# Kernel tuning notes

Measured on AMD Instinct MI355X. Metric: run time of the kernel, lower is better.

## Reference

```python
import jax, jax.numpy as jnp
import numpy as np

H = 128  # GRU hidden size


def _conv(x, w, b, stride):
    # x: NCHW, w: OIHW, VALID padding (torch Conv2d default padding=0)
    y = jax.lax.conv_general_dilated(x, w, (stride, stride), 'VALID',
                                     dimension_numbers=('NCHW', 'OIHW', 'NCHW'))
    return y + b[None, :, None, None]


def setup_inputs() -> dict:
    key = jax.random.key(0)
    ks = jax.random.split(key, 16)
    T, B, A = 128, 32, 6
    x = jax.random.uniform(ks[0], (T * B, 1, 84, 84), jnp.float32) * 255.0
    done = (jax.random.uniform(ks[1], (T * B,)) < 0.1).astype(jnp.float32)
    gru_state = jnp.zeros((1, B, H), jnp.float32)
    s = 0.05
    params = dict(
        conv1_w=jax.random.normal(ks[2], (32, 1, 8, 8)) * s,
        conv1_b=jnp.zeros((32,)),
        conv2_w=jax.random.normal(ks[3], (64, 32, 4, 4)) * s,
        conv2_b=jnp.zeros((64,)),
        conv3_w=jax.random.normal(ks[4], (64, 64, 3, 3)) * s,
        conv3_b=jnp.zeros((64,)),
        fc_w=jax.random.normal(ks[5], (512, 64 * 7 * 7)) * 0.02,
        fc_b=jnp.zeros((512,)),
        w_ih=jax.random.normal(ks[6], (3 * H, 512)) * 0.04,
        w_hh=jax.random.normal(ks[7], (3 * H, H)) * 0.08,
        b_ih=jnp.zeros((3 * H,)),
        b_hh=jnp.zeros((3 * H,)),
        actor_w=jax.random.normal(ks[8], (A, H)) * 0.01,
        actor_b=jnp.zeros((A,)),
        critic_w=jax.random.normal(ks[9], (1, H)) * 0.09,
        critic_b=jnp.zeros((1,)),
    )
    return dict(x=x, done=done, gru_state=gru_state, **params)


def reference(x, done, gru_state,
              conv1_w, conv1_b, conv2_w, conv2_b, conv3_w, conv3_b,
              fc_w, fc_b, w_ih, w_hh, b_ih, b_hh,
              actor_w, actor_b, critic_w, critic_b):
    # CNN encoder on x/255
    h = jax.nn.relu(_conv(x / 255.0, conv1_w, conv1_b, 4))  # [N,32,20,20]
    h = jax.nn.relu(_conv(h, conv2_w, conv2_b, 2))          # [N,64,9,9]
    h = jax.nn.relu(_conv(h, conv3_w, conv3_b, 1))          # [N,64,7,7]
    feat = jax.nn.relu(h.reshape(h.shape[0], -1) @ fc_w.T + fc_b)  # [N,512]

    B = gru_state.shape[1]
    feat = feat.reshape(-1, B, feat.shape[-1])  # [T,B,512]
    d = done.reshape(-1, B)                     # [T,B]

    # hoist input-to-gate projection out of the scan
    gx = jnp.einsum('tbi,gi->tbg', feat, w_ih) + b_ih  # [T,B,3H]

    def step(hprev, inp):
        gxt, dt = inp
        hprev = (1.0 - dt)[:, None] * hprev  # done-reset mask
        gh = hprev @ w_hh.T + b_hh           # [B,3H]
        r = jax.nn.sigmoid(gxt[:, :H] + gh[:, :H])
        z = jax.nn.sigmoid(gxt[:, H:2 * H] + gh[:, H:2 * H])
        n = jnp.tanh(gxt[:, 2 * H:] + r * gh[:, 2 * H:])
        hnew = (1.0 - z) * n + z * hprev
        return hnew, hnew

    h_final, hs = jax.lax.scan(step, gru_state[0], (gx, d))
    hidden = hs.reshape(-1, H)  # [T*B,H]

    logits = hidden @ actor_w.T + actor_b   # [N,A]
    value = hidden @ critic_w.T + critic_b  # [N,1]
    return logits, value, h_final[None]
```

## Files before the change

### kernel.cpp

```cpp
#include <hip/hip_runtime.h>
#include <hip/hip_bf16.h>
#include <stdint.h>

#define DI __device__ __forceinline__

typedef __bf16 bf16x8 __attribute__((ext_vector_type(8)));
typedef __bf16 bf16x4 __attribute__((ext_vector_type(4)));
typedef float f32x16 __attribute__((ext_vector_type(16)));

DI float bf2f(unsigned short u){ return __uint_as_float(((unsigned int)u)<<16); }
DI unsigned short f2bf(float f){
  unsigned int x = __float_as_uint(f);
  x += 0x7fffu + ((x>>16)&1u);
  return (unsigned short)(x>>16);
}
DI float sigmoidf_(float x){ return 1.0f/(1.0f + __expf(-x)); }

DI void gld_lds16(const void* g, void* l){
  __builtin_amdgcn_global_load_lds((const __attribute__((address_space(1))) void*)g,
                                   (__attribute__((address_space(3))) void*)l, 16, 0, 0);
}
DI f32x16 mfma32(bf16x8 a, bf16x8 b, f32x16 c){
  return __builtin_amdgcn_mfma_f32_32x32x16_bf16(a, b, c, 0, 0, 0);
}

__global__ __launch_bounds__(256) void k_prep_w1(const float* __restrict__ w1, unsigned short* __restrict__ o){
  int idx = blockIdx.x*256 + threadIdx.x;
  int j=idx&7, l=(idx>>3)&63, kk=idx>>9;
  int oc=l&31, kg=kk*16+((l>>5)<<3)+j;
  o[idx] = f2bf(w1[oc*64 + kg] * (1.0f/255.0f));
}
__global__ __launch_bounds__(256) void k_prep_w2(const float* __restrict__ w2, unsigned short* __restrict__ o){
  int idx = blockIdx.x*256 + threadIdx.x;
  int j=idx&7, l=(idx>>3)&63, nt=(idx>>9)&1, kh=(idx>>10)&1, s=idx>>11;
  int oc=nt*32+(l&31), ic=kh*16+(l>>5)*8+j, ky=s>>2, kx=s&3;
  o[idx] = f2bf(w2[((oc*32+ic)*4+ky)*4+kx]);
}
__global__ __launch_bounds__(256) void k_prep_w3(const float* __restrict__ w3, unsigned short* __restrict__ o){
  int idx = blockIdx.x*256 + threadIdx.x;
  int j=idx&7, l=(idx>>3)&63, nt=(idx>>9)&1, kh=(idx>>10)&3, s=idx>>12;
  int oc=nt*32+(l&31), ic=kh*16+(l>>5)*8+j, ky=s/3, kx=s-ky*3;
  o[idx] = f2bf(w3[((oc*64+ic)*3+ky)*3+kx]);
}
__global__ __launch_bounds__(512) void k_prep_fc(const float* __restrict__ fcw, unsigned short* __restrict__ o){
  int tid=threadIdx.x, ks=blockIdx.x, nt=blockIdx.y;
  int j=tid&7, l=tid>>3;
  int n=nt*32+(l&31), k=ks*16+(l>>5)*8+j;
  int c=k&63, pos=k>>6;
  float wv = fcw[(size_t)n*3136 + c*49 + pos];
  unsigned short hi = f2bf(wv);
  int idx = (nt*196+ks)*512 + tid;
  o[idx] = hi;
  o[1605632 + idx] = f2bf(wv - bf2f(hi));
}
__global__ __launch_bounds__(512) void k_prep_gx(const float* __restrict__ wih, unsigned short* __restrict__ o){
  int tid=threadIdx.x, ks=blockIdx.x, nt=blockIdx.y;
  int j=tid&7, l=tid>>3;
  int n=nt*32+(l&31), k=ks*16+(l>>5)*8+j;
  float wv = wih[(size_t)n*512 + k];
  unsigned short hi = f2bf(wv);
  int idx = (nt*32+ks)*512 + tid;
  o[idx] = hi;
  o[196608 + idx] = f2bf(wv - bf2f(hi));
}

__global__ __launch_bounds__(256) void k_conv1(const float* __restrict__ x,
    const unsigned short* __restrict__ w1p, const float* __restrict__ b,
    unsigned short* __restrict__ a1, int nbase)
{
  __shared__ __align__(16) char imgs[4*14784];
  const int tid=threadIdx.x, l=tid&63, w=tid>>6;
  const int nloc = blockIdx.x*4 + w;
  char* myimg = imgs + w*14784;
  const float* xp = x + (size_t)(nbase+nloc)*7056;

  for (int it=0; it<28; ++it){
    int idx4 = l + it*64;
    if (idx4 < 1764){
      float4 v = *(const float4*)(xp + idx4*4);
      int row = idx4/21, rem = idx4 - row*21;
      ushort4 u; u.x=f2bf(v.x); u.y=f2bf(v.y); u.z=f2bf(v.z); u.w=f2bf(v.w);
      *(ushort4*)(myimg + row*176 + rem*8) = u;
    }
  }

  bf16x8 wb[4];
  #pragma unroll
  for (int kk=0;kk<4;kk++) wb[kk] = *(const bf16x8*)(w1p + (kk*64 + l)*8);
  const float bias = b[l&31];
  asm volatile("s_waitcnt lgkmcnt(0)" ::: "memory");

  const int kyh = (l>>5);
  unsigned short* obase = a1 + (size_t)nloc*12800;
  for (int mt=0; mt<13; ++mt){
    int p = mt*32 + (l&31);
    p = min(p, 399);
    const int oy = p/20, ox = p - oy*20;
    const int rbyte = oy*4*176 + ox*8;
    f32x16 acc = {};
    #pragma unroll
    for (int kk=0;kk<4;kk++){
      const int a = rbyte + (kk*2 + kyh)*176;
      bf16x8 af;
      *(bf16x4*)&af       = *(const bf16x4*)(myimg + a);
      *((bf16x4*)&af + 1) = *(const bf16x4*)(myimg + a + 8);
      acc = mfma32(af, wb[kk], acc);
    }
    const int oc = l&31;
    #pragma unroll
    for (int rg=0;rg<16;rg++){
      int row = (rg&3) + 8*(rg>>2) + 4*kyh;
      int pos = mt*32 + row;
      if (pos < 400)
        obase[pos*32 + oc] = f2bf(fmaxf(acc[rg] + bias, 0.f));
    }
  }
}

__global__ __launch_bounds__(256) void k_conv2(const unsigned short* __restrict__ a1,
    const unsigned short* __restrict__ w2p, const float* __restrict__ b2,
    unsigned short* __restrict__ a2, int nbase)
{
  extern __shared__ __align__(16) char smem[];
  const int tid=threadIdx.x, l=tid&63, w=tid>>6;
  const int nloc = blockIdx.x*4 + w;
  char* myimg = smem + w*25600;
  const char* gimg = (const char*)(a1 + (size_t)nloc*12800);
  #pragma unroll
  for (int i=0;i<25;i++){
    int o = i*1024 + l*16;
    int q = o ^ (((o>>7)&7)<<4);
    gld_lds16(gimg + q, myimg + i*1024);
  }
  __syncthreads();
  int rbase[3];
  #pragma unroll
  for (int mt=0;mt<3;mt++){
    int r = mt*32 + (l&31);
    int oy=r/9, ox=r-oy*9;
    rbase[mt] = 40*oy + 2*ox;
  }
  const int grp16 = (l>>5)*16;
  f32x16 acc[3][2] = {};
  #pragma unroll
  for (int ky=0;ky<4;ky++){
    #pragma unroll
    for (int kx=0;kx<4;kx++){
      const int s = ky*4+kx;
      #pragma unroll
      for (int kh=0;kh<2;kh++){
        bf16x8 b0 = *(const bf16x8*)(w2p + (((s*2+kh)*2+0)*64 + l)*8);
        bf16x8 b1 = *(const bf16x8*)(w2p + (((s*2+kh)*2+1)*64 + l)*8);
        #pragma unroll
        for (int mt=0;mt<3;mt++){
          int ip = rbase[mt] + ky*20 + kx;
          ip = min(ip, 399);
          int byte = (ip*64 + kh*32 + grp16) ^ (((ip>>1)&7)<<4);
          bf16x8 af = *(const bf16x8*)(myimg + byte);
          acc[mt][0] = mfma32(af, b0, acc[mt][0]);
          acc[mt][1] = mfma32(af, b1, acc[mt][1]);
        }
      }
    }
  }
  const float bias0 = b2[l&31], bias1 = b2[32+(l&31)];
  unsigned short* ob = (unsigned short*)myimg;
  #pragma unroll
  for (int mt=0;mt<3;mt++){
    #pragma unroll
    for (int rg=0;rg<16;rg++){
      int r = mt*32 + (rg&3) + 8*(rg>>2) + 4*(l>>5);
      ob[r*64 + (l&31)]      = f2bf(fmaxf(acc[mt][0][rg]+bias0,0.f));
      ob[r*64 + 32 + (l&31)] = f2bf(fmaxf(acc[mt][1][rg]+bias1,0.f));
    }
  }
  asm volatile("s_waitcnt lgkmcnt(0)" ::: "memory");
  const uint4* s4 = (const uint4*)ob;
  uint4* d4 = (uint4*)(a2 + (size_t)(nbase+nloc)*5184);
  #pragma unroll
  for (int i=0;i<11;i++){
    int c = i*64 + l;
    if (c < 648) d4[c] = s4[c];
  }
}

__global__ __launch_bounds__(256) void k_conv3(const unsigned short* __restrict__ a2,
    const unsigned short* __restrict__ w3p, const float* __restrict__ b3,
    unsigned short* __restrict__ a3)
{
  __shared__ __align__(16) char smem3[4*11264];
  const int tid=threadIdx.x, l=tid&63, w=tid>>6;
  const int n = blockIdx.x*4 + w;
  char* myimg = smem3 + w*11264;
  const char* gimg = (const char*)(a2 + (size_t)n*5184);
  #pragma unroll
  for (int i=0;i<11;i++){
    int c = i*64 + l;
    int cc = min(c, 647);
    int o = cc*16;
    int q = o ^ (((o>>7)&7)<<4);
    gld_lds16(gimg + q, myimg + i*1024);
  }
  __syncthreads();
  int base[2];
  #pragma unroll
  for (int mt=0;mt<2;mt++){
    int r = mt*32 + (l&31);
    int oy=r/7, ox=r-oy*7;
    base[mt] = oy*9 + ox;
  }
  const int grp16 = (l>>5)*16;
  f32x16 acc[2][2] = {};
  #pragma unroll
  for (int ky=0;ky<3;ky++){
    #pragma unroll
    for (int kx=0;kx<3;kx++){
      const int s = ky*3+kx;
      #pragma unroll
      for (int kh=0;kh<4;kh++){
        bf16x8 b0 = *(const bf16x8*)(w3p + (((s*4+kh)*2+0)*64 + l)*8);
        bf16x8 b1 = *(const bf16x8*)(w3p + (((s*4+kh)*2+1)*64 + l)*8);
        #pragma unroll
        for (int mt=0;mt<2;mt++){
          int ip = min(base[mt] + ky*9 + kx, 80);
          int byte = (ip*128 + kh*32 + grp16) ^ ((ip&7)<<4);
          bf16x8 af = *(const bf16x8*)(myimg + byte);
          acc[mt][0] = mfma32(af, b0, acc[mt][0]);
          acc[mt][1] = mfma32(af, b1, acc[mt][1]);
        }
      }
    }
  }
  const float bias0 = b3[l&31], bias1 = b3[32+(l&31)];
  unsigned short* ob = (unsigned short*)myimg;
  #pragma unroll
  for (int mt=0;mt<2;mt++){
    #pragma unroll
    for (int rg=0;rg<16;rg++){
      int r = mt*32 + (rg&3) + 8*(rg>>2) + 4*(l>>5);
      if (r < 49){
        ob[r*64 + (l&31)]      = f2bf(fmaxf(acc[mt][0][rg]+bias0,0.f));
        ob[r*64 + 32 + (l&31)] = f2bf(fmaxf(acc[mt][1][rg]+bias1,0.f));
      }
    }
  }
  asm volatile("s_waitcnt lgkmcnt(0)" ::: "memory");
  const uint4* s4 = (const uint4*)ob;
  uint4* d4 = (uint4*)(a3 + (size_t)n*3136);
  #pragma unroll
  for (int i=0;i<7;i++){
    int c = i*64 + l;
    if (c < 392) d4[c] = s4[c];
  }
}

template<bool RELU, bool OBF16>
__global__ __launch_bounds__(256) void k_gemm(const unsigned short* __restrict__ A, int K,
    const unsigned short* __restrict__ Wp, int loOff, const float* __restrict__ bias,
    void* __restrict__ out, int N)
{
  __shared__ __align__(16) char ab[2][8192];
  const int tid=threadIdx.x, l=tid&63, w=tid>>6;
  const int m0=blockIdx.y*128, n0=blockIdx.x*64;
  const int KS=K>>4, T=K>>5;
  const int mh=w&1, ntl=w>>1;
  const int ntg = blockIdx.x*2 + ntl;
  const char* Ab = (const char*)A;

  f32x16 acc[2] = {};
  bf16x8 bh0, bh1, bl0, bl1, nh0, nh1, nl0, nl1;

  #pragma unroll
  for (int i=0;i<2;i++){
    int o = (w*2+i)*1024 + l*16;
    int q = o ^ (((o>>7)&7)<<4);
    int row = q>>6, kc=(q>>4)&3;
    gld_lds16(Ab + ((size_t)(m0+row)*K)*2 + kc*16, ab[0] + (w*2+i)*1024);
  }
  {
    const unsigned short* p0 = Wp + ((size_t)(ntg*KS)*64 + l)*8;
    bh0 = *(const bf16x8*)(p0);
    bh1 = *(const bf16x8*)(p0 + 512);
    bl0 = *(const bf16x8*)(p0 + loOff);
    bl1 = *(const bf16x8*)(p0 + loOff + 512);
  }
  __syncthreads();

  for (int t=0;t<T;t++){
    const int cb = t&1;
    if (t+1 < T){
      #pragma unroll
      for (int i=0;i<2;i++){
        int o = (w*2+i)*1024 + l*16;
        int q = o ^ (((o>>7)&7)<<4);
        int row = q>>6, kc=(q>>4)&3;
        gld_lds16(Ab + ((size_t)(m0+row)*K + (t+1)*32)*2 + kc*16, ab[cb^1] + (w*2+i)*1024);
      }
      const unsigned short* pn = Wp + ((size_t)(ntg*KS + (t+1)*2)*64 + l)*8;
      nh0 = *(const bf16x8*)(pn);
      nh1 = *(const bf16x8*)(pn + 512);
      nl0 = *(const bf16x8*)(pn + loOff);
      nl1 = *(const bf16x8*)(pn + loOff + 512);
    }
    #pragma unroll
    for (int mt=0;mt<2;mt++){
      int r = mh*64 + mt*32 + (l&31);
      int b0 = (r*64 + (l>>5)*16) ^ (((r>>1)&7)<<4);
      bf16x8 a0 = *(const bf16x8*)(ab[cb] + b0);
      bf16x8 a1 = *(const bf16x8*)(ab[cb] + (b0^32));
      acc[mt] = mfma32(a0, bh0, acc[mt]);
      acc[mt] = mfma32(a1, bh1, acc[mt]);
      acc[mt] = mfma32(a0, bl0, acc[mt]);
      acc[mt] = mfma32(a1, bl1, acc[mt]);
    }
    __syncthreads();
    bh0=nh0; bh1=nh1; bl0=nl0; bl1=nl1;
  }

  const int col = n0 + ntl*32 + (l&31);
  const float bv = bias[col];
  #pragma unroll
  for (int mt=0;mt<2;mt++){
    #pragma unroll
    for (int rg=0;rg<16;rg++){
      int r = m0 + mh*64 + mt*32 + (rg&3) + 8*(rg>>2) + 4*(l>>5);
      float v = acc[mt][rg] + bv;
      if (RELU) v = fmaxf(v, 0.f);
      if (OBF16) ((unsigned short*)out)[(size_t)r*N + col] = f2bf(v);
      else       ((float*)out)[(size_t)r*N + col] = v;
    }
  }
}

__global__ __launch_bounds__(512) void k_gru(const float* __restrict__ gx,
    const float* __restrict__ done, const float* __restrict__ h0,
    const float* __restrict__ whh, const float* __restrict__ bhh,
    float* __restrict__ hid, float* __restrict__ hfin)
{
  __shared__ __align__(16) float hs[128];
  const int b = blockIdx.x, tid = threadIdx.x;
  const int u = tid>>2, sub = tid&3;
  float wr[32], wz[32], wn[32];
  const float* wru = whh + (size_t)u*128 + sub*32;
  const float* wzu = whh + (size_t)(u+128)*128 + sub*32;
  const float* wnu = whh + (size_t)(u+256)*128 + sub*32;
  #pragma unroll
  for (int i=0;i<8;i++){
    *(float4*)&wr[i*4] = *(const float4*)(wru+i*4);
    *(float4*)&wz[i*4] = *(const float4*)(wzu+i*4);
    *(float4*)&wn[i*4] = *(const float4*)(wnu+i*4);
  }
  const float br = bhh[u], bz = bhh[u+128], bn = bhh[u+256];
  if (tid<128) hs[tid] = h0[(size_t)b*128+tid];
  for (int t=0;t<128;t++){
    __syncthreads();
    const float keep = 1.0f - done[t*32+b];
    float hv[32];
    #pragma unroll
    for (int i=0;i<8;i++) *(float4*)&hv[i*4] = *(const float4*)&hs[sub*32+i*4];
    float ar=0.f, az=0.f, an=0.f;
    #pragma unroll
    for (int i=0;i<32;i++){
      ar = fmaf(wr[i],hv[i],ar);
      az = fmaf(wz[i],hv[i],az);
      an = fmaf(wn[i],hv[i],an);
    }
    ar += __shfl_xor(ar,1); ar += __shfl_xor(ar,2);
    az += __shfl_xor(az,1); az += __shfl_xor(az,2);
    an += __shfl_xor(an,1); an += __shfl_xor(an,2);
    float hn = 0.f;
    if (sub==0){
      const float hp = keep*hs[u];
      const float* gxr = gx + ((size_t)t*32+b)*384;
      const float r  = sigmoidf_(gxr[u]     + keep*ar + br);
      const float z  = sigmoidf_(gxr[u+128] + keep*az + bz);
      const float nn = tanhf   (gxr[u+256] + r*(keep*an + bn));
      hn = (1.0f-z)*nn + z*hp;
      hid[((size_t)t*32+b)*128 + u] = hn;
    }
    __syncthreads();
    if (sub==0) hs[u]=hn;
  }
  __syncthreads();
  if (tid<128) hfin[(size_t)b*128+tid]=hs[tid];
}

__global__ __launch_bounds__(256) void k_heads(const float* __restrict__ hid,
    const float* __restrict__ aw, const float* __restrict__ ab,
    const float* __restrict__ cw, const float* __restrict__ cb,
    float* __restrict__ out)
{
  __shared__ __align__(16) float wsm[7*128];
  __shared__ float bb[7];
  const int tid = threadIdx.x;
  for (int i=tid;i<896;i+=256) wsm[i] = (i<768) ? aw[i] : cw[i-768];
  if (tid<7) bb[tid] = (tid<6) ? ab[tid] : cb[0];
  __syncthreads();
  const int idx = blockIdx.x*256 + tid;
  const int n = idx/7, a = idx - n*7;
  const float4* hp = (const float4*)(hid + (size_t)n*128);
  const float4* wp = (const float4*)(&wsm[a*128]);
  float s = bb[a];
  #pragma unroll
  for (int q=0;q<32;q++){
    const float4 h4=hp[q], w4=wp[q];
    s += h4.x*w4.x + h4.y*w4.y + h4.z*w4.z + h4.w*w4.w;
  }
  if (a<6) out[(size_t)n*6+a]=s; else out[24576+n]=s;
}

extern "C" void kernel_launch(void* const* d_in, const int* in_sizes, int n_in,
                              void* d_out, int out_size, void* d_ws, size_t ws_size,
                              hipStream_t stream)
{
  const float* x    = (const float*)d_in[0];
  const float* done = (const float*)d_in[1];
  const float* h0   = (const float*)d_in[2];
  const float* c1w  = (const float*)d_in[3];
  const float* c1b  = (const float*)d_in[4];
  const float* c2w  = (const float*)d_in[5];
  const float* c2b  = (const float*)d_in[6];
  const float* c3w  = (const float*)d_in[7];
  const float* c3b  = (const float*)d_in[8];
  const float* fcw  = (const float*)d_in[9];
  const float* fcb  = (const float*)d_in[10];
  const float* wih  = (const float*)d_in[11];
  const float* whh  = (const float*)d_in[12];
  const float* bih  = (const float*)d_in[13];
  const float* bhh  = (const float*)d_in[14];
  const float* aw   = (const float*)d_in[15];
  const float* ab   = (const float*)d_in[16];
  const float* cw   = (const float*)d_in[17];
  const float* cb   = (const float*)d_in[18];
  float* out = (float*)d_out;
  char* ws = (char*)d_ws;

  unsigned short* W1P  = (unsigned short*)(ws);
  unsigned short* W2P  = (unsigned short*)(ws + 4096);
  unsigned short* W3P  = (unsigned short*)(ws + 69632);
  unsigned short* FCWP = (unsigned short*)(ws + 143360);
  unsigned short* GXWP = (unsigned short*)(ws + 6565888);
  unsigned short* A1   = (unsigned short*)(ws + 7352320);
  unsigned short* A2   = (unsigned short*)(ws + 59781120);
  unsigned short* A3   = (unsigned short*)(ws + 7352320);
  unsigned short* FEAT = (unsigned short*)(ws + 33042432);
  float* GX   = (float*)(ws + 37236736);
  float* HID  = (float*)(ws + 43528192);

  static bool attr_set = false;
  if (!attr_set) {
    (void)hipFuncSetAttribute((const void*)k_conv2, hipFuncAttributeMaxDynamicSharedMemorySize, 102400);
    attr_set = true;
  }

  k_prep_w1<<<8, 256, 0, stream>>>(c1w, W1P);
  k_prep_w2<<<128, 256, 0, stream>>>(c2w, W2P);
  k_prep_w3<<<144, 256, 0, stream>>>(c3w, W3P);
  k_prep_fc<<<dim3(196,16), 512, 0, stream>>>(fcw, FCWP);
  k_prep_gx<<<dim3(32,12), 512, 0, stream>>>(wih, GXWP);

  for (int pass=0; pass<2; pass++){
    k_conv1<<<512, 256, 0, stream>>>(x, W1P, c1b, A1, pass*2048);
    k_conv2<<<512, 256, 102400, stream>>>(A1, W2P, c2b, A2, pass*2048);
  }
  k_conv3<<<1024, 256, 0, stream>>>(A2, W3P, c3b, A3);
  k_gemm<true, true ><<<dim3(8,32), 256, 0, stream>>>(A3, 3136, FCWP, 1605632, fcb, (void*)FEAT, 512);
  k_gemm<false,false><<<dim3(6,32), 256, 0, stream>>>(FEAT, 512, GXWP, 196608, bih, (void*)GX, 384);
  k_gru<<<32, 512, 0, stream>>>(GX, done, h0, whh, bhh, HID, out + 28672);
  k_heads<<<112, 256, 0, stream>>>(HID, aw, ab, cw, cb, out);
}
```

Before: 386.4 us.

## Double-buffer GRU hidden state, prefetch gate inputs, use packed FMA and fast tanh

The GRU recurrence kernel now ping-pongs the hidden state between two shared buffers, which drops one barrier per timestep. It also prefetches the next step's gate inputs and done flag into registers so their global latency overlaps the current step. The matvec uses two-wide float vectors so the compiler can emit packed FMAs, the shared-memory reads are rotated per lane to spread bank access, and tanhf is replaced with an exp-based formula. The exp-based tanh gives slightly different numerics, and the extra prefetch registers raise register pressure.

Measured after the change: 1.239 ms. 3.21x slower.

```diff
diff --git a/kernel.cpp b/kernel.cpp
--- a/kernel.cpp
+++ b/kernel.cpp
@@ -7,6 +7,7 @@
 typedef __bf16 bf16x8 __attribute__((ext_vector_type(8)));
 typedef __bf16 bf16x4 __attribute__((ext_vector_type(4)));
 typedef float f32x16 __attribute__((ext_vector_type(16)));
+typedef float f32x2 __attribute__((ext_vector_type(2)));
 
 DI float bf2f(unsigned short u){ return __uint_as_float(((unsigned int)u)<<16); }
 DI unsigned short f2bf(float f){
@@ -15,6 +16,7 @@
   return (unsigned short)(x>>16);
 }
 DI float sigmoidf_(float x){ return 1.0f/(1.0f + __expf(-x)); }
+DI float tanhf_(float x){ return 2.0f/(1.0f + __expf(-2.0f*x)) - 1.0f; }
 
 DI void gld_lds16(const void* g, void* l){
   __builtin_amdgcn_global_load_lds((const __attribute__((address_space(1))) void*)g,
@@ -337,52 +339,68 @@
     const float* __restrict__ whh, const float* __restrict__ bhh,
     float* __restrict__ hid, float* __restrict__ hfin)
 {
-  __shared__ __align__(16) float hs[128];
+  __shared__ __align__(16) float hs[2][128];
   const int b = blockIdx.x, tid = threadIdx.x;
   const int u = tid>>2, sub = tid&3;
-  float wr[32], wz[32], wn[32];
+  f32x2 wr[16], wz[16], wn[16];
   const float* wru = whh + (size_t)u*128 + sub*32;
   const float* wzu = whh + (size_t)(u+128)*128 + sub*32;
   const float* wnu = whh + (size_t)(u+256)*128 + sub*32;
   #pragma unroll
   for (int i=0;i<8;i++){
-    *(float4*)&wr[i*4] = *(const float4*)(wru+i*4);
-    *(float4*)&wz[i*4] = *(const float4*)(wzu+i*4);
-    *(float4*)&wn[i*4] = *(const float4*)(wnu+i*4);
+    *(float4*)&wr[i*2] = *(const float4*)(wru+i*4);
+    *(float4*)&wz[i*2] = *(const float4*)(wzu+i*4);
+    *(float4*)&wn[i*2] = *(const float4*)(wnu+i*4);
   }
   const float br = bhh[u], bz = bhh[u+128], bn = bhh[u+256];
-  if (tid<128) hs[tid] = h0[(size_t)b*128+tid];
+  if (tid<128) hs[0][tid] = h0[(size_t)b*128+tid];
+
+  const float* g0 = gx + (size_t)b*384;
+  float pg0 = g0[u], pg1 = g0[u+128], pg2 = g0[u+256];
+  float pd  = done[b];
+  __syncthreads();
+
   for (int t=0;t<128;t++){
-    __syncthreads();
-    const float keep = 1.0f - done[t*32+b];
-    float hv[32];
-    #pragma unroll
-    for (int i=0;i<8;i++) *(float4*)&hv[i*4] = *(const float4*)&hs[sub*32+i*4];
-    float ar=0.f, az=0.f, an=0.f;
-    #pragma unroll
-    for (int i=0;i<32;i++){
-      ar = fmaf(wr[i],hv[i],ar);
-      az = fmaf(wz[i],hv[i],az);
-      an = fmaf(wn[i],hv[i],an);
-    }
+    const int cur = t&1;
+    const float gr=pg0, gz=pg1, gn=pg2, dn=pd;
+    if (t+1 < 128){
+      const float* gp = gx + ((size_t)(t+1)*32+b)*384;
+      pg0=gp[u]; pg1=gp[u+128]; pg2=gp[u+256];
+      pd = done[(t+1)*32+b];
+    }
+    const float* hb = &hs[cur][sub*32];
+    f32x2 hv[16];
+    #pragma unroll
+    for (int q=0;q<8;q++){
+      const int e = (q + sub*2)&7;
+      float4 v = *(const float4*)(hb + e*4);
+      hv[e*2]   = *(f32x2*)&v.x;
+      hv[e*2+1] = *(f32x2*)&v.z;
+    }
+    f32x2 a2r = {0.f,0.f}, a2z = {0.f,0.f}, a2n = {0.f,0.f};
+    #pragma unroll
+    for (int i=0;i<16;i++){
+      a2r += wr[i]*hv[i];
+      a2z += wz[i]*hv[i];
+      a2n += wn[i]*hv[i];
+    }
+    float ar=a2r[0]+a2r[1], az=a2z[0]+a2z[1], an=a2n[0]+a2n[1];
     ar += __shfl_xor(ar,1); ar += __shfl_xor(ar,2);
     az += __shfl_xor(az,1); az += __shfl_xor(az,2);
     an += __shfl_xor(an,1); an += __shfl_xor(an,2);
-    float hn = 0.f;
     if (sub==0){
-      const float hp = keep*hs[u];
-      const float* gxr = gx + ((size_t)t*32+b)*384;
-      const float r  = sigmoidf_(gxr[u]     + keep*ar + br);
-      const float z  = sigmoidf_(gxr[u+128] + keep*az + bz);
-      const float nn = tanhf   (gxr[u+256] + r*(keep*an + bn));
-      hn = (1.0f-z)*nn + z*hp;
+      const float keep = 1.0f - dn;
+      const float hp = keep*hs[cur][u];
+      const float r  = sigmoidf_(gr + keep*ar + br);
+      const float z  = sigmoidf_(gz + keep*az + bz);
+      const float nn = tanhf_  (gn + r*(keep*an + bn));
+      const float hn = (1.0f-z)*nn + z*hp;
       hid[((size_t)t*32+b)*128 + u] = hn;
+      hs[cur^1][u] = hn;
     }
     __syncthreads();
-    if (sub==0) hs[u]=hn;
-  }
-  __syncthreads();
-  if (tid<128) hfin[(size_t)b*128+tid]=hs[tid];
+  }
+  if (tid<128) hfin[(size_t)b*128+tid] = hs[0][tid];
 }
 
 __global__ __launch_bounds__(256) void k_heads(const float* __restrict__ hid,
```
